# Kernel optimization log

Measured on AMD Instinct MI355X. Metric: run time of the kernel, lower is better.

Reference implementation:

```python
import jax, jax.numpy as jnp
import numpy as np

N = 100000   # nodes per graph-set
E = 600000   # edges
G = 64       # graphs in batch
H = 128      # hidden size (atom_h == voro_h == embeddings)
STEPS = 4
F_B = 90     # atom feature length
F_V = 20     # voro feature length


def setup_inputs() -> dict:
    key = jax.random.key(0)
    ks = jax.random.split(key, 16)
    inp = {
        "x_b": jax.random.uniform(ks[0], (N, F_B), dtype=jnp.float32),
        "edge_index_b": jax.random.randint(ks[1], (2, E), 0, N, dtype=jnp.int32),
        "batch_b": jnp.sort(jax.random.randint(ks[2], (N,), 0, G, dtype=jnp.int32)),
        "x_v": jax.random.uniform(ks[3], (N, F_V), dtype=jnp.float32),
        "edge_index_v": jax.random.randint(ks[4], (2, E), 0, N, dtype=jnp.int32),
        "batch_v": jnp.sort(jax.random.randint(ks[5], (N,), 0, G, dtype=jnp.int32)),
        # embedding linears (bias=False)
        "W_emb_b": jax.random.normal(ks[6], (F_B, H), dtype=jnp.float32) * 0.05,
        "W_emb_v": jax.random.normal(ks[7], (F_V, H), dtype=jnp.float32) * 0.05,
        # GatedGraphConv (the *bond* block — source applies it to both graphs)
        "ggc_weight": jax.random.normal(ks[8], (STEPS, H, H), dtype=jnp.float32) * 0.05,
        "gru_w_ih": jax.random.normal(ks[9], (3 * H, H), dtype=jnp.float32) * 0.05,
        "gru_w_hh": jax.random.normal(ks[10], (3 * H, H), dtype=jnp.float32) * 0.05,
        "gru_b_ih": jnp.zeros((3 * H,), dtype=jnp.float32),
        "gru_b_hh": jnp.zeros((3 * H,), dtype=jnp.float32),
        # output block (hidden = 2H)
        "W1": jax.random.normal(ks[11], (2 * H, 2 * H), dtype=jnp.float32) * 0.05,
        "b1": jnp.zeros((2 * H,), dtype=jnp.float32),
        "W2": jax.random.normal(ks[12], (2 * H, 1), dtype=jnp.float32) * 0.05,
        "b2": jnp.zeros((1,), dtype=jnp.float32),
    }
    return inp


def _gru_cell(m, h, w_ih, w_hh, b_ih, b_hh):
    gi = m @ w_ih.T + b_ih   # [N, 3H]
    gh = h @ w_hh.T + b_hh
    i_r, i_z, i_n = jnp.split(gi, 3, axis=-1)
    h_r, h_z, h_n = jnp.split(gh, 3, axis=-1)
    r = jax.nn.sigmoid(i_r + h_r)
    z = jax.nn.sigmoid(i_z + h_z)
    n = jnp.tanh(i_n + r * h_n)
    return (1.0 - z) * n + z * h


def _gated_graph_conv(x, edge_index, ggc_weight, gru_w_ih, gru_w_hh, gru_b_ih, gru_b_hh):
    # x: [N, H] (in_channels == out_channels, no padding needed)
    src, dst = edge_index[0], edge_index[1]
    h = x
    for i in range(STEPS):
        m = h @ ggc_weight[i]                                   # [N, H]
        agg = jax.ops.segment_sum(m[src], dst, num_segments=N)  # add-aggregation
        h = _gru_cell(agg, h, gru_w_ih, gru_w_hh, gru_b_ih, gru_b_hh)
    return h


def _mean_pool(x, batch):
    sums = jax.ops.segment_sum(x, batch, num_segments=G)
    cnt = jax.ops.segment_sum(jnp.ones((x.shape[0],), x.dtype), batch, num_segments=G)
    return sums / jnp.maximum(cnt, 1.0)[:, None]


def reference(x_b, edge_index_b, batch_b, x_v, edge_index_v, batch_v,
              W_emb_b, W_emb_v, ggc_weight, gru_w_ih, gru_w_hh, gru_b_ih, gru_b_hh,
              W1, b1, W2, b2):
    # embedding blocks: relu(linear(x)) (no bias)
    hb = jax.nn.relu(x_b @ W_emb_b)
    hv = jax.nn.relu(x_v @ W_emb_v)
    # NOTE: source (faithfully) applies mpnn_layer_bond to BOTH graphs
    hb = _gated_graph_conv(hb, edge_index_b, ggc_weight, gru_w_ih, gru_w_hh, gru_b_ih, gru_b_hh)
    hv = _gated_graph_conv(hv, edge_index_v, ggc_weight, gru_w_ih, gru_w_hh, gru_b_ih, gru_b_hh)
    gb = _mean_pool(jax.nn.relu(hb), batch_b)   # [G, H]
    gv = _mean_pool(jax.nn.relu(hv), batch_v)   # [G, H]
    g = jnp.concatenate([gb, gv], axis=1)       # [G, 2H]
    out = jax.nn.softplus(jax.nn.relu(g @ W1 + b1) @ W2 + b2)
    return out.squeeze(1)                       # [G]
```

## Files before the change

### kernel.cpp

```cpp
#include <hip/hip_runtime.h>
#include <hip/hip_bf16.h>
#include <math.h>

#define N_NODES   100000
#define N_EDGES   600000
#define NG        64
#define H         128
#define STEPS     4
#define FB        90
#define FV        20
#define NN        (2*N_NODES)
#define EE        (2*N_EDGES)
#define BSTR      40
#define NBLK      196
#define NNP       (NBLK*1024)

#define WCAT_KC   (12*64*8)
#define WCAT_HALF (8*WCAT_KC)
#define WCAT_STEP (2*WCAT_HALF)

typedef unsigned short u16;
typedef __attribute__((ext_vector_type(8))) __bf16 bf16x8;
typedef __attribute__((ext_vector_type(4))) float  floatx4;

static __device__ __forceinline__ float bf16_lo(unsigned u){ return __uint_as_float(u << 16); }
static __device__ __forceinline__ float bf16_hi(unsigned u){ return __uint_as_float(u & 0xffff0000u); }
static __device__ __forceinline__ u16 f2bf(float f){
    union { float f; unsigned u; } v; v.f = f;
    unsigned r = v.u + 0x7fffu + ((v.u >> 16) & 1u);
    return (u16)(r >> 16);
}
static __device__ __forceinline__ float fastrcp(float x){ return __builtin_amdgcn_rcpf(x); }
static __device__ __forceinline__ float fsigmoid(float x){ return fastrcp(1.f + __expf(-x)); }
static __device__ __forceinline__ float ftanh(float x){ return 1.f - 2.f*fastrcp(1.f + __expf(2.f*x)); }


__global__ void deg_kernel(const int* __restrict__ eib, const int* __restrict__ eiv,
                           int* __restrict__ deg){
    int e = blockIdx.x*blockDim.x + threadIdx.x;
    if (e >= EE) return;
    int d;
    if (e < N_EDGES) d = eib[N_EDGES + e];
    else             d = eiv[N_EDGES + (e - N_EDGES)] + N_NODES;
    atomicAdd(&deg[d], 1);
}

__global__ __launch_bounds__(256) void bsum_kernel(const int* __restrict__ deg, int* __restrict__ bsum){
    int t = threadIdx.x;
    int4 v = reinterpret_cast<const int4*>(deg)[blockIdx.x*256 + t];
    int s = v.x + v.y + v.z + v.w;
    __shared__ int ss[256];
    ss[t] = s; __syncthreads();
    for (int off = 128; off > 0; off >>= 1){ if (t < off) ss[t] += ss[t + off]; __syncthreads(); }
    if (t == 0) bsum[blockIdx.x] = ss[0];
}

__global__ __launch_bounds__(256) void bscan_kernel(const int* __restrict__ bsum, int* __restrict__ boff){
    int t = threadIdx.x;
    int v = (t < NBLK) ? bsum[t] : 0;
    __shared__ int ss[256];
    ss[t] = v; __syncthreads();
    for (int off = 1; off < 256; off <<= 1){
        int u = (t >= off) ? ss[t - off] : 0;
        __syncthreads();
        ss[t] += u;
        __syncthreads();
    }
    boff[t] = ss[t] - v;
}

__global__ __launch_bounds__(256) void scan_final_kernel(const int* __restrict__ deg, const int* __restrict__ boff,
                                                         int* __restrict__ row_ptr, int* __restrict__ cursor){
    int t = threadIdx.x, b = blockIdx.x;
    int4 v = reinterpret_cast<const int4*>(deg)[b*256 + t];
    int s = v.x + v.y + v.z + v.w;
    __shared__ int ss[256];
    ss[t] = s; __syncthreads();
    for (int off = 1; off < 256; off <<= 1){
        int u = (t >= off) ? ss[t - off] : 0;
        __syncthreads();
        ss[t] += u;
        __syncthreads();
    }
    int base = boff[b] + ss[t] - s;
    int i0 = b*1024 + t*4;
    int e0 = base, e1 = e0 + v.x, e2 = e1 + v.y, e3 = e2 + v.z;
    if (i0 < NN){
        int4 w = make_int4(e0, e1, e2, e3);
        reinterpret_cast<int4*>(row_ptr)[i0 >> 2] = w;
        reinterpret_cast<int4*>(cursor)[i0 >> 2]  = w;
    }
    if (b == 0 && t == 0) row_ptr[NN] = EE;
}

__global__ void csr_fill_kernel(const int* __restrict__ eib, const int* __restrict__ eiv,
                                int* __restrict__ cursor, int* __restrict__ csr_src){
    int e = blockIdx.x*blockDim.x + threadIdx.x;
    if (e >= EE) return;
    int s, d;
    if (e < N_EDGES){ s = eib[e];                 d = eib[N_EDGES + e]; }
    else { int e2 = e - N_EDGES; s = eiv[e2] + N_NODES; d = eiv[N_EDGES + e2] + N_NODES; }
    int pos = atomicAdd(&cursor[d], 1);
    csr_src[pos] = s;
}

__global__ __launch_bounds__(128) void fold_kernel(const float* __restrict__ ggc_w,
                                                   const float* __restrict__ w_ih,
                                                   float* __restrict__ Bfold){
    int blk = blockIdx.x;
    int s = blk >> 7, k = blk & 127;
    __shared__ float wg[128];
    int t = threadIdx.x;
    wg[t] = ggc_w[(size_t)s*H*H + (size_t)k*H + t];
    __syncthreads();
    for (int c = t; c < 384; c += 128){
        const float* wr = w_ih + (size_t)c*H;
        float acc = 0.f;
        for (int q = 0; q < 128; q += 4){
            float4 a = *reinterpret_cast<const float4*>(&wg[q]);
            float4 b = *reinterpret_cast<const float4*>(&wr[q]);
            acc += a.x*b.x + a.y*b.y + a.z*b.z + a.w*b.w;
        }
        Bfold[((size_t)s*H + k)*384 + c] = acc;
    }
}

__global__ void pack_kernel(const float* __restrict__ Bfold, const float* __restrict__ w_hh,
                            u16* __restrict__ Wcat){
    int idx = blockIdx.x*256 + threadIdx.x;
    if (idx >= STEPS*WCAT_STEP) return;
    int v    = idx & 7;
    int lane = (idx >> 3) & 63;
    int t    = (idx >> 9) % 12;
    int rem  = idx / (512*12);
    int kc   = rem & 7;
    int b1   = (rem >> 3) & 1;
    int s    = rem >> 4;
    int col16 = lane & 15, l4 = lane >> 4;
    int k = kc*32 + l4*8 + v;
    int g = t >> 2, jj = t & 3;
    int c = (4*b1 + jj)*16 + col16;
    int gc = (g == 2) ? (256 + c) : (g*128 + c);
    float val;
    if (k < 128) val = Bfold[((size_t)s*H + k)*384 + gc];
    else         val = w_hh[(size_t)gc*H + (k - 128)];
    Wcat[idx] = f2bf(val);
}


__global__ __launch_bounds__(128) void emb_kernel(const float* __restrict__ xb, const float* __restrict__ xv,
                                                  const float* __restrict__ Wb, const float* __restrict__ Wv,
                                                  u16* __restrict__ hb){
    __shared__ float xs[8][FB];
    int j = threadIdx.x;
    int n0 = blockIdx.x * 8;
    const float* x; const float* W; int K; int xoff;
    if (n0 < N_NODES){ x = xb; W = Wb; K = FB; xoff = n0; }
    else             { x = xv; W = Wv; K = FV; xoff = n0 - N_NODES; }
    for (int i = j; i < 8*K; i += 128){ int r = i / K, c = i - r*K; xs[r][c] = x[(xoff + r)*K + c]; }
    __syncthreads();
    float acc[8];
    #pragma unroll
    for (int n = 0; n < 8; ++n) acc[n] = 0.f;
    for (int k = 0; k < K; ++k){
        float w = W[k*H + j];
        #pragma unroll
        for (int n = 0; n < 8; ++n) acc[n] = fmaf(xs[n][k], w, acc[n]);
    }
    #pragma unroll
    for (int n = 0; n < 8; ++n)
        hb[(size_t)(n0 + n)*H + j] = f2bf(fmaxf(acc[n], 0.f));
}


__global__ __launch_bounds__(256) void agg_kernel(const u16* __restrict__ hb,
                                                  const int* __restrict__ row_ptr,
                                                  const int* __restrict__ csr_src,
                                                  u16* __restrict__ aggb){
    int wid  = threadIdx.x >> 6;
    int lane = threadIdx.x & 63;
    int q    = lane >> 4;
    int c    = lane & 15;
    int node = blockIdx.x*4 + wid;
    int beg = row_ptr[node], end = row_ptr[node+1];
    const uint4* rows = reinterpret_cast<const uint4*>(hb);
    float s0=0.f,s1=0.f,s2=0.f,s3=0.f,s4=0.f,s5=0.f,s6=0.f,s7=0.f;
    float u0=0.f,u1=0.f,u2=0.f,u3=0.f,u4=0.f,u5=0.f,u6=0.f,u7=0.f;
    int e = beg + q;
    for (; e + 4 < end; e += 8){
        int sA = csr_src[e];
        int sB = csr_src[e + 4];
        uint4 a = rows[(size_t)sA*16 + c];
        uint4 b = rows[(size_t)sB*16 + c];
        s0 += bf16_lo(a.x); s1 += bf16_hi(a.x); s2 += bf16_lo(a.y); s3 += bf16_hi(a.y);
        s4 += bf16_lo(a.z); s5 += bf16_hi(a.z); s6 += bf16_lo(a.w); s7 += bf16_hi(a.w);
        u0 += bf16_lo(b.x); u1 += bf16_hi(b.x); u2 += bf16_lo(b.y); u3 += bf16_hi(b.y);
        u4 += bf16_lo(b.z); u5 += bf16_hi(b.z); u6 += bf16_lo(b.w); u7 += bf16_hi(b.w);
    }
    if (e < end){
        int sA = csr_src[e];
        uint4 a = rows[(size_t)sA*16 + c];
        s0 += bf16_lo(a.x); s1 += bf16_hi(a.x); s2 += bf16_lo(a.y); s3 += bf16_hi(a.y);
        s4 += bf16_lo(a.z); s5 += bf16_hi(a.z); s6 += bf16_lo(a.w); s7 += bf16_hi(a.w);
    }
    s0 += u0; s1 += u1; s2 += u2; s3 += u3; s4 += u4; s5 += u5; s6 += u6; s7 += u7;
    s0 += __shfl_xor(s0, 16); s1 += __shfl_xor(s1, 16); s2 += __shfl_xor(s2, 16); s3 += __shfl_xor(s3, 16);
    s4 += __shfl_xor(s4, 16); s5 += __shfl_xor(s5, 16); s6 += __shfl_xor(s6, 16); s7 += __shfl_xor(s7, 16);
    s0 += __shfl_xor(s0, 32); s1 += __shfl_xor(s1, 32); s2 += __shfl_xor(s2, 32); s3 += __shfl_xor(s3, 32);
    s4 += __shfl_xor(s4, 32); s5 += __shfl_xor(s5, 32); s6 += __shfl_xor(s6, 32); s7 += __shfl_xor(s7, 32);
    if (q == 0){
        uint4 o;
        o.x = (unsigned)f2bf(s0) | ((unsigned)f2bf(s1) << 16);
        o.y = (unsigned)f2bf(s2) | ((unsigned)f2bf(s3) << 16);
        o.z = (unsigned)f2bf(s4) | ((unsigned)f2bf(s5) << 16);
        o.w = (unsigned)f2bf(s6) | ((unsigned)f2bf(s7) << 16);
        reinterpret_cast<uint4*>(aggb)[(size_t)node*16 + c] = o;
    }
}


__global__ __launch_bounds__(256, 3) void gru_mfma_kernel(const u16* __restrict__ aggb,
                                                          const u16* __restrict__ hb_in,
                                                          u16* __restrict__ hb_out,
                                                          const u16* __restrict__ Wcat,
                                                          const float* __restrict__ b_ih,
                                                          const float* __restrict__ b_hh){
    __shared__ u16 Bs[WCAT_KC];
    __shared__ u16 As[64*BSTR];
    const int t = threadIdx.x;
    const int wid = t >> 6, lane = t & 63;
    const int l15 = lane & 15, l4 = lane >> 4;
    const int n0 = blockIdx.x * 64;
    const int b1 = blockIdx.y;
    const u16* Wsrc = Wcat + (size_t)b1*WCAT_HALF;

    floatx4 accR[4], accZ[4], accNi[4], accNh[4];
    #pragma unroll
    for (int i = 0; i < 4; ++i){
        accR[i] = (floatx4){0.f,0.f,0.f,0.f};  accZ[i]  = (floatx4){0.f,0.f,0.f,0.f};
        accNi[i] = (floatx4){0.f,0.f,0.f,0.f}; accNh[i] = (floatx4){0.f,0.f,0.f,0.f};
    }

    for (int kc = 0; kc < 8; ++kc){
        __syncthreads();
        {
            const u16* src = Wsrc + (size_t)kc*WCAT_KC;
#if __has_builtin(__builtin_amdgcn_global_load_lds)
            #pragma unroll
            for (int p = 0; p < 3; ++p){
                int i = t + p*256;
                __builtin_amdgcn_global_load_lds(
                    (const __attribute__((address_space(1))) void*)(src + (size_t)i*8),
                    (__attribute__((address_space(3))) void*)(&Bs[i*8]), 16, 0, 0);
            }
#else
            #pragma unroll
            for (int p = 0; p < 3; ++p){
                int i = t + p*256;
                *reinterpret_cast<int4*>(&Bs[i*8]) = *reinterpret_cast<const int4*>(src + (size_t)i*8);
            }
#endif
        }
        {
            int row = t >> 2, part = t & 3;
            const u16* srcA = (kc < 4) ? aggb : hb_in;
            const int4 v = *reinterpret_cast<const int4*>(srcA + (size_t)(n0 + row)*H + (kc & 3)*32 + part*8);
            *reinterpret_cast<int4*>(&As[row*BSTR + part*8]) = v;
        }
        __syncthreads();
        bf16x8 aF = *reinterpret_cast<const bf16x8*>(&As[(wid*16 + l15)*BSTR + l4*8]);
        if (kc < 4){
            #pragma unroll
            for (int j = 0; j < 4; ++j){
                bf16x8 bR = *reinterpret_cast<const bf16x8*>(&Bs[((0*4 + j)*64 + lane)*8]);
                bf16x8 bZ = *reinterpret_cast<const bf16x8*>(&Bs[((1*4 + j)*64 + lane)*8]);
                bf16x8 bN = *reinterpret_cast<const bf16x8*>(&Bs[((2*4 + j)*64 + lane)*8]);
                accR[j]  = __builtin_amdgcn_mfma_f32_16x16x32_bf16(aF, bR, accR[j], 0, 0, 0);
                accZ[j]  = __builtin_amdgcn_mfma_f32_16x16x32_bf16(aF, bZ, accZ[j], 0, 0, 0);
                accNi[j] = __builtin_amdgcn_mfma_f32_16x16x32_bf16(aF, bN, accNi[j], 0, 0, 0);
            }
        } else {
            #pragma unroll
            for (int j = 0; j < 4; ++j){
                bf16x8 bR = *reinterpret_cast<const bf16x8*>(&Bs[((0*4 + j)*64 + lane)*8]);
                bf16x8 bZ = *reinterpret_cast<const bf16x8*>(&Bs[((1*4 + j)*64 + lane)*8]);
                bf16x8 bN = *reinterpret_cast<const bf16x8*>(&Bs[((2*4 + j)*64 + lane)*8]);
                accR[j]  = __builtin_amdgcn_mfma_f32_16x16x32_bf16(aF, bR, accR[j], 0, 0, 0);
                accZ[j]  = __builtin_amdgcn_mfma_f32_16x16x32_bf16(aF, bZ, accZ[j], 0, 0, 0);
                accNh[j] = __builtin_amdgcn_mfma_f32_16x16x32_bf16(aF, bN, accNh[j], 0, 0, 0);
            }
        }
    }

    const int rowb = n0 + wid*16 + l4*4;
    #pragma unroll
    for (int jj = 0; jj < 4; ++jj){
        int col = (4*b1 + jj)*16 + l15;
        float br  = b_ih[col]       + b_hh[col];
        float bz  = b_ih[128 + col] + b_hh[128 + col];
        float bin = b_ih[256 + col];
        float bhn = b_hh[256 + col];
        #pragma unroll
        for (int rg = 0; rg < 4; ++rg){
            int row = rowb + rg;
            float r   = fsigmoid(accR[jj][rg] + br);
            float z   = fsigmoid(accZ[jj][rg] + bz);
            float nn_ = ftanh(accNi[jj][rg] + bin + r*(accNh[jj][rg] + bhn));
            float hold = bf16_lo((unsigned)hb_in[(size_t)row*H + col]);
            float hnew = (1.f - z)*nn_ + z*hold;
            hb_out[(size_t)row*H + col] = f2bf(hnew);
        }
    }
}


__global__ __launch_bounds__(128) void pool_kernel(const u16* __restrict__ hb,
                                                   const int* __restrict__ batch_b, const int* __restrict__ batch_v,
                                                   float* __restrict__ pool){
    int j  = threadIdx.x;
    int n0 = blockIdx.x * 32;
    bool voro = (n0 >= N_NODES);
    int colbase = voro ? 128 : 0;
    int gcur = -1; float acc = 0.f;
    for (int r = 0; r < 32; ++r){
        int node = n0 + r;
        int g = voro ? batch_v[node - N_NODES] : batch_b[node];
        if (g != gcur){
            if (gcur >= 0) atomicAdd(&pool[gcur*256 + colbase + j], acc);
            acc = 0.f; gcur = g;
        }
        acc += fmaxf(bf16_lo((unsigned)hb[(size_t)node*H + j]), 0.f);
    }
    if (gcur >= 0) atomicAdd(&pool[gcur*256 + colbase + j], acc);
}

__global__ __launch_bounds__(256) void cnt_kernel(const int* __restrict__ batch_b, const int* __restrict__ batch_v,
                                                  int* __restrict__ cnt){
    __shared__ int bins[128];
    int t = threadIdx.x;
    if (t < 128) bins[t] = 0;
    __syncthreads();
    int i = blockIdx.x*256 + t;
    if (i < NN){
        int g = (i < N_NODES) ? batch_b[i] : 64 + batch_v[i - N_NODES];
        atomicAdd(&bins[g], 1);
    }
    __syncthreads();
    if (t < 128 && bins[t] > 0) atomicAdd(&cnt[t], bins[t]);
}


__global__ __launch_bounds__(256) void head_kernel(const float* __restrict__ pool, const int* __restrict__ cnt,
                                                   const float* __restrict__ W1, const float* __restrict__ b1,
                                                   const float* __restrict__ W2, const float* __restrict__ b2,
                                                   float* __restrict__ out){
    __shared__ float gs[256];
    __shared__ float wsum[4];
    int b = blockIdx.x, j = threadIdx.x;
    int c = (j < 128) ? cnt[b] : cnt[64 + b];
    float denom = (float)((c > 1) ? c : 1);
    gs[j] = pool[b*256 + j] / denom;
    __syncthreads();
    float acc = b1[j];
    for (int k = 0; k < 256; ++k) acc = fmaf(gs[k], W1[k*256 + j], acc);
    float y = fmaxf(acc, 0.f) * W2[j];
    #pragma unroll
    for (int off = 32; off > 0; off >>= 1) y += __shfl_down(y, off, 64);
    if ((j & 63) == 0) wsum[j >> 6] = y;
    __syncthreads();
    if (j == 0){
        float x = wsum[0] + wsum[1] + wsum[2] + wsum[3] + b2[0];
        float sp = (x > 0.f) ? x + log1pf(expf(-x)) : log1pf(expf(x));
        out[b] = sp;
    }
}


extern "C" void kernel_launch(void* const* d_in, const int* in_sizes, int n_in,
                              void* d_out, int out_size, void* d_ws, size_t ws_size,
                              hipStream_t stream){
    const float* x_b      = (const float*)d_in[0];
    const int*   eib      = (const int*)  d_in[1];
    const int*   batch_b  = (const int*)  d_in[2];
    const float* x_v      = (const float*)d_in[3];
    const int*   eiv      = (const int*)  d_in[4];
    const int*   batch_v  = (const int*)  d_in[5];
    const float* W_emb_b  = (const float*)d_in[6];
    const float* W_emb_v  = (const float*)d_in[7];
    const float* ggc_w    = (const float*)d_in[8];
    const float* gru_w_ih = (const float*)d_in[9];
    const float* gru_w_hh = (const float*)d_in[10];
    const float* gru_b_ih = (const float*)d_in[11];
    const float* gru_b_hh = (const float*)d_in[12];
    const float* W1       = (const float*)d_in[13];
    const float* b1       = (const float*)d_in[14];
    const float* W2       = (const float*)d_in[15];
    const float* b2       = (const float*)d_in[16];
    float* out = (float*)d_out;

    char* ws = (char*)d_ws;
    size_t off = 0;
    auto alloc = [&](size_t bytes)->char*{
        char* p = ws + off; off += (bytes + 255)/256*256; return p;
    };
    u16*   hb0      = (u16*)   alloc((size_t)NN*H*2);
    u16*   hb1      = (u16*)   alloc((size_t)NN*H*2);
    u16*   aggb     = (u16*)   alloc((size_t)NN*H*2);
    float* Bfold    = (float*) alloc((size_t)STEPS*H*384*4);
    u16*   Wcat     = (u16*)   alloc((size_t)STEPS*WCAT_STEP*2);
    int*   row_ptr  = (int*)   alloc((size_t)(NN+1)*4);
    int*   deg      = (int*)   alloc((size_t)NNP*4);
    int*   cursor   = (int*)   alloc((size_t)NN*4);
    int*   csr_src  = (int*)   alloc((size_t)EE*4);
    int*   bsum     = (int*)   alloc((size_t)256*4);
    int*   boff     = (int*)   alloc((size_t)256*4);
    float* pool     = (float*) alloc((size_t)NG*2*H*4);
    int*   cnt      = (int*)   alloc((size_t)2*NG*4);
    (void)ws_size; (void)in_sizes; (void)n_in; (void)out_size;

    hipMemsetAsync(deg,  0, (size_t)NNP*4, stream);
    hipMemsetAsync(pool, 0, (size_t)NG*2*H*4, stream);
    hipMemsetAsync(cnt,  0, (size_t)2*NG*4, stream);

    deg_kernel        <<<(EE + 255)/256, 256, 0, stream>>>(eib, eiv, deg);
    bsum_kernel       <<<NBLK, 256, 0, stream>>>(deg, bsum);
    bscan_kernel      <<<1, 256, 0, stream>>>(bsum, boff);
    scan_final_kernel <<<NBLK, 256, 0, stream>>>(deg, boff, row_ptr, cursor);
    csr_fill_kernel   <<<(EE + 255)/256, 256, 0, stream>>>(eib, eiv, cursor, csr_src);
    fold_kernel       <<<STEPS*H, 128, 0, stream>>>(ggc_w, gru_w_ih, Bfold);
    pack_kernel       <<<(STEPS*WCAT_STEP + 255)/256, 256, 0, stream>>>(Bfold, gru_w_hh, Wcat);

    emb_kernel<<<NN/8, 128, 0, stream>>>(x_b, x_v, W_emb_b, W_emb_v, hb0);

    u16* hbs[2] = { hb0, hb1 };
    for (int s = 0; s < STEPS; ++s){
        u16* hin  = hbs[s & 1];
        u16* hout = hbs[(s + 1) & 1];
        agg_kernel     <<<NN/4, 256, 0, stream>>>(hin, row_ptr, csr_src, aggb);
        gru_mfma_kernel<<<dim3(NN/64, 2), 256, 0, stream>>>(aggb, hin, hout,
                                                            Wcat + (size_t)s*WCAT_STEP,
                                                            gru_b_ih, gru_b_hh);
    }

    pool_kernel<<<NN/32, 128, 0, stream>>>(hb0, batch_b, batch_v, pool);
    cnt_kernel <<<(NN + 255)/256, 256, 0, stream>>>(batch_b, batch_v, cnt);
    head_kernel<<<NG, 256, 0, stream>>>(pool, cnt, W1, b1, W2, b2, out);
}
```

Baseline: 955.7 us.

## Fuse neighbor aggregation into GRU MFMA kernel via shared memory

```diff
diff --git a/kernel.cpp b/kernel.cpp
--- a/kernel.cpp
+++ b/kernel.cpp
@@ -11,9 +11,9 @@
 #define FV        20
 #define NN        (2*N_NODES)
 #define EE        (2*N_EDGES)
-#define BSTR      40
 #define NBLK      196
 #define NNP       (NBLK*1024)
+#define AGSTR     136
 
 #define WCAT_KC   (12*64*8)
 #define WCAT_HALF (8*WCAT_KC)
@@ -173,66 +173,72 @@
 }
 
 
-__global__ __launch_bounds__(256) void agg_kernel(const u16* __restrict__ hb,
-                                                  const int* __restrict__ row_ptr,
-                                                  const int* __restrict__ csr_src,
-                                                  u16* __restrict__ aggb){
-    int wid  = threadIdx.x >> 6;
-    int lane = threadIdx.x & 63;
-    int q    = lane >> 4;
-    int c    = lane & 15;
-    int node = blockIdx.x*4 + wid;
-    int beg = row_ptr[node], end = row_ptr[node+1];
-    const uint4* rows = reinterpret_cast<const uint4*>(hb);
-    float s0=0.f,s1=0.f,s2=0.f,s3=0.f,s4=0.f,s5=0.f,s6=0.f,s7=0.f;
-    float u0=0.f,u1=0.f,u2=0.f,u3=0.f,u4=0.f,u5=0.f,u6=0.f,u7=0.f;
-    int e = beg + q;
-    for (; e + 4 < end; e += 8){
-        int sA = csr_src[e];
-        int sB = csr_src[e + 4];
-        uint4 a = rows[(size_t)sA*16 + c];
-        uint4 b = rows[(size_t)sB*16 + c];
-        s0 += bf16_lo(a.x); s1 += bf16_hi(a.x); s2 += bf16_lo(a.y); s3 += bf16_hi(a.y);
-        s4 += bf16_lo(a.z); s5 += bf16_hi(a.z); s6 += bf16_lo(a.w); s7 += bf16_hi(a.w);
-        u0 += bf16_lo(b.x); u1 += bf16_hi(b.x); u2 += bf16_lo(b.y); u3 += bf16_hi(b.y);
-        u4 += bf16_lo(b.z); u5 += bf16_hi(b.z); u6 += bf16_lo(b.w); u7 += bf16_hi(b.w);
-    }
-    if (e < end){
-        int sA = csr_src[e];
-        uint4 a = rows[(size_t)sA*16 + c];
-        s0 += bf16_lo(a.x); s1 += bf16_hi(a.x); s2 += bf16_lo(a.y); s3 += bf16_hi(a.y);
-        s4 += bf16_lo(a.z); s5 += bf16_hi(a.z); s6 += bf16_lo(a.w); s7 += bf16_hi(a.w);
-    }
-    s0 += u0; s1 += u1; s2 += u2; s3 += u3; s4 += u4; s5 += u5; s6 += u6; s7 += u7;
-    s0 += __shfl_xor(s0, 16); s1 += __shfl_xor(s1, 16); s2 += __shfl_xor(s2, 16); s3 += __shfl_xor(s3, 16);
-    s4 += __shfl_xor(s4, 16); s5 += __shfl_xor(s5, 16); s6 += __shfl_xor(s6, 16); s7 += __shfl_xor(s7, 16);
-    s0 += __shfl_xor(s0, 32); s1 += __shfl_xor(s1, 32); s2 += __shfl_xor(s2, 32); s3 += __shfl_xor(s3, 32);
-    s4 += __shfl_xor(s4, 32); s5 += __shfl_xor(s5, 32); s6 += __shfl_xor(s6, 32); s7 += __shfl_xor(s7, 32);
-    if (q == 0){
-        uint4 o;
-        o.x = (unsigned)f2bf(s0) | ((unsigned)f2bf(s1) << 16);
-        o.y = (unsigned)f2bf(s2) | ((unsigned)f2bf(s3) << 16);
-        o.z = (unsigned)f2bf(s4) | ((unsigned)f2bf(s5) << 16);
-        o.w = (unsigned)f2bf(s6) | ((unsigned)f2bf(s7) << 16);
-        reinterpret_cast<uint4*>(aggb)[(size_t)node*16 + c] = o;
-    }
-}
-
-
-__global__ __launch_bounds__(256, 3) void gru_mfma_kernel(const u16* __restrict__ aggb,
-                                                          const u16* __restrict__ hb_in,
-                                                          u16* __restrict__ hb_out,
-                                                          const u16* __restrict__ Wcat,
-                                                          const float* __restrict__ b_ih,
-                                                          const float* __restrict__ b_hh){
-    __shared__ u16 Bs[WCAT_KC];
-    __shared__ u16 As[64*BSTR];
+__global__ __launch_bounds__(512, 4) void step_kernel(const u16* __restrict__ hb_in,
+                                                      u16* __restrict__ hb_out,
+                                                      const int* __restrict__ row_ptr,
+                                                      const int* __restrict__ csr_src,
+                                                      const u16* __restrict__ Wcat,
+                                                      const float* __restrict__ b_ih,
+                                                      const float* __restrict__ b_hh){
+    __shared__ u16 AggS[64*AGSTR];
+    __shared__ u16 HbS [64*AGSTR];
+    __shared__ u16 Bs  [2*WCAT_KC];
     const int t = threadIdx.x;
     const int wid = t >> 6, lane = t & 63;
     const int l15 = lane & 15, l4 = lane >> 4;
+    const int w4  = wid & 3;
+    const int b1h = wid >> 2;
     const int n0 = blockIdx.x * 64;
-    const int b1 = blockIdx.y;
-    const u16* Wsrc = Wcat + (size_t)b1*WCAT_HALF;
+
+    {
+        #pragma unroll
+        for (int p = 0; p < 2; ++p){
+            int i = t + p*512;
+            int row = i >> 4, part = i & 15;
+            const int4 v = *reinterpret_cast<const int4*>(hb_in + (size_t)(n0 + row)*H + part*8);
+            *reinterpret_cast<int4*>(&HbS[row*AGSTR + part*8]) = v;
+        }
+    }
+    {
+        int q = lane >> 4, c = lane & 15;
+        const uint4* rows = reinterpret_cast<const uint4*>(hb_in);
+        for (int it = 0; it < 8; ++it){
+            int node = n0 + wid*8 + it;
+            int beg = row_ptr[node], end = row_ptr[node+1];
+            float s0=0.f,s1=0.f,s2=0.f,s3=0.f,s4=0.f,s5=0.f,s6=0.f,s7=0.f;
+            float u0=0.f,u1=0.f,u2=0.f,u3=0.f,u4=0.f,u5=0.f,u6=0.f,u7=0.f;
+            int e = beg + q;
+            for (; e + 4 < end; e += 8){
+                int sA = csr_src[e];
+                int sB = csr_src[e + 4];
+                uint4 a = rows[(size_t)sA*16 + c];
+                uint4 b = rows[(size_t)sB*16 + c];
+                s0 += bf16_lo(a.x); s1 += bf16_hi(a.x); s2 += bf16_lo(a.y); s3 += bf16_hi(a.y);
+                s4 += bf16_lo(a.z); s5 += bf16_hi(a.z); s6 += bf16_lo(a.w); s7 += bf16_hi(a.w);
+                u0 += bf16_lo(b.x); u1 += bf16_hi(b.x); u2 += bf16_lo(b.y); u3 += bf16_hi(b.y);
+                u4 += bf16_lo(b.z); u5 += bf16_hi(b.z); u6 += bf16_lo(b.w); u7 += bf16_hi(b.w);
+            }
+            if (e < end){
+                int sA = csr_src[e];
+                uint4 a = rows[(size_t)sA*16 + c];
+                s0 += bf16_lo(a.x); s1 += bf16_hi(a.x); s2 += bf16_lo(a.y); s3 += bf16_hi(a.y);
+                s4 += bf16_lo(a.z); s5 += bf16_hi(a.z); s6 += bf16_lo(a.w); s7 += bf16_hi(a.w);
+            }
+            s0 += u0; s1 += u1; s2 += u2; s3 += u3; s4 += u4; s5 += u5; s6 += u6; s7 += u7;
+            s0 += __shfl_xor(s0, 16); s1 += __shfl_xor(s1, 16); s2 += __shfl_xor(s2, 16); s3 += __shfl_xor(s3, 16);
+            s4 += __shfl_xor(s4, 16); s5 += __shfl_xor(s5, 16); s6 += __shfl_xor(s6, 16); s7 += __shfl_xor(s7, 16);
+            s0 += __shfl_xor(s0, 32); s1 += __shfl_xor(s1, 32); s2 += __shfl_xor(s2, 32); s3 += __shfl_xor(s3, 32);
+            s4 += __shfl_xor(s4, 32); s5 += __shfl_xor(s5, 32); s6 += __shfl_xor(s6, 32); s7 += __shfl_xor(s7, 32);
+            if (q == 0){
+                uint4 o;
+                o.x = (unsigned)f2bf(s0) | ((unsigned)f2bf(s1) << 16);
+                o.y = (unsigned)f2bf(s2) | ((unsigned)f2bf(s3) << 16);
+                o.z = (unsigned)f2bf(s4) | ((unsigned)f2bf(s5) << 16);
+                o.w = (unsigned)f2bf(s6) | ((unsigned)f2bf(s7) << 16);
+                *reinterpret_cast<uint4*>(&AggS[(wid*8 + it)*AGSTR + c*8]) = o;
+            }
+        }
+    }
 
     floatx4 accR[4], accZ[4], accNi[4], accNh[4];
     #pragma unroll
@@ -244,37 +250,36 @@
     for (int kc = 0; kc < 8; ++kc){
         __syncthreads();
         {
-            const u16* src = Wsrc + (size_t)kc*WCAT_KC;
+            const u16* src = Wcat + (size_t)kc*WCAT_KC;
 #if __has_builtin(__builtin_amdgcn_global_load_lds)
             #pragma unroll
             for (int p = 0; p < 3; ++p){
-                int i = t + p*256;
+                int i = t + p*512;
+                int half = (i >= 768), idx = i - half*768;
                 __builtin_amdgcn_global_load_lds(
-                    (const __attribute__((address_space(1))) void*)(src + (size_t)i*8),
-                    (__attribute__((address_space(3))) void*)(&Bs[i*8]), 16, 0, 0);
+                    (const __attribute__((address_space(1))) void*)(src + (size_t)half*WCAT_HALF + (size_t)idx*8),
+                    (__attribute__((address_space(3))) void*)(&Bs[(half*768 + idx)*8]), 16, 0, 0);
             }
 #else
             #pragma unroll
             for (int p = 0; p < 3; ++p){
-                int i = t + p*256;
-                *reinterpret_cast<int4*>(&Bs[i*8]) = *reinterpret_cast<const int4*>(src + (size_t)i*8);
+                int i = t + p*512;
+                int half = (i >= 768), idx = i - half*768;
+                *reinterpret_cast<int4*>(&Bs[(half*768 + idx)*8]) =
+                    *reinterpret_cast<const int4*>(src + (size_t)half*WCAT_HALF + (size_t)idx*8);
             }
 #endif
         }
-        {
-            int row = t >> 2, part = t & 3;
-            const u16* srcA = (kc < 4) ? aggb : hb_in;
-            const int4 v = *reinterpret_cast<const int4*>(srcA + (size_t)(n0 + row)*H + (kc & 3)*32 + part*8);
-            *reinterpret_cast<int4*>(&As[row*BSTR + part*8]) = v;
-        }
-        __syncthreads();
-        bf16x8 aF = *reinterpret_cast<const bf16x8*>(&As[(wid*16 + l15)*BSTR + l4*8]);
+        __syncthreads();
+        const u16* Asrc = (kc < 4) ? AggS : HbS;
+        bf16x8 aF = *reinterpret_cast<const bf16x8*>(&Asrc[(w4*16 + l15)*AGSTR + (kc & 3)*32 + l4*8]);
+        const u16* Bh = &Bs[b1h*WCAT_KC];
         if (kc < 4){
             #pragma unroll
             for (int j = 0; j < 4; ++j){
-                bf16x8 bR = *reinterpret_cast<const bf16x8*>(&Bs[((0*4 + j)*64 + lane)*8]);
-                bf16x8 bZ = *reinterpret_cast<const bf16x8*>(&Bs[((1*4 + j)*64 + lane)*8]);
-                bf16x8 bN = *reinterpret_cast<const bf16x8*>(&Bs[((2*4 + j)*64 + lane)*8]);
+                bf16x8 bR = *reinterpret_cast<const bf16x8*>(&Bh[((0*4 + j)*64 + lane)*8]);
+                bf16x8 bZ = *reinterpret_cast<const bf16x8*>(&Bh[((1*4 + j)*64 + lane)*8]);
+                bf16x8 bN = *reinterpret_cast<const bf16x8*>(&Bh[((2*4 + j)*64 + lane)*8]);
                 accR[j]  = __builtin_amdgcn_mfma_f32_16x16x32_bf16(aF, bR, accR[j], 0, 0, 0);
                 accZ[j]  = __builtin_amdgcn_mfma_f32_16x16x32_bf16(aF, bZ, accZ[j], 0, 0, 0);
                 accNi[j] = __builtin_amdgcn_mfma_f32_16x16x32_bf16(aF, bN, accNi[j], 0, 0, 0);
@@ -282,9 +287,9 @@
         } else {
             #pragma unroll
             for (int j = 0; j < 4; ++j){
-                bf16x8 bR = *reinterpret_cast<const bf16x8*>(&Bs[((0*4 + j)*64 + lane)*8]);
-                bf16x8 bZ = *reinterpret_cast<const bf16x8*>(&Bs[((1*4 + j)*64 + lane)*8]);
-                bf16x8 bN = *reinterpret_cast<const bf16x8*>(&Bs[((2*4 + j)*64 + lane)*8]);
+                bf16x8 bR = *reinterpret_cast<const bf16x8*>(&Bh[((0*4 + j)*64 + lane)*8]);
+                bf16x8 bZ = *reinterpret_cast<const bf16x8*>(&Bh[((1*4 + j)*64 + lane)*8]);
+                bf16x8 bN = *reinterpret_cast<const bf16x8*>(&Bh[((2*4 + j)*64 + lane)*8]);
                 accR[j]  = __builtin_amdgcn_mfma_f32_16x16x32_bf16(aF, bR, accR[j], 0, 0, 0);
                 accZ[j]  = __builtin_amdgcn_mfma_f32_16x16x32_bf16(aF, bZ, accZ[j], 0, 0, 0);
                 accNh[j] = __builtin_amdgcn_mfma_f32_16x16x32_bf16(aF, bN, accNh[j], 0, 0, 0);
@@ -292,10 +297,10 @@
         }
     }
 
-    const int rowb = n0 + wid*16 + l4*4;
+    const int rowb = n0 + w4*16 + l4*4;
     #pragma unroll
     for (int jj = 0; jj < 4; ++jj){
-        int col = (4*b1 + jj)*16 + l15;
+        int col = (4*b1h + jj)*16 + l15;
         float br  = b_ih[col]       + b_hh[col];
         float bz  = b_ih[128 + col] + b_hh[128 + col];
         float bin = b_ih[256 + col];
@@ -306,7 +311,7 @@
             float r   = fsigmoid(accR[jj][rg] + br);
             float z   = fsigmoid(accZ[jj][rg] + bz);
             float nn_ = ftanh(accNi[jj][rg] + bin + r*(accNh[jj][rg] + bhn));
-            float hold = bf16_lo((unsigned)hb_in[(size_t)row*H + col]);
+            float hold = bf16_lo((unsigned)HbS[(row - n0)*AGSTR + col]);
             float hnew = (1.f - z)*nn_ + z*hold;
             hb_out[(size_t)row*H + col] = f2bf(hnew);
         }
@@ -405,7 +410,6 @@
     };
     u16*   hb0      = (u16*)   alloc((size_t)NN*H*2);
     u16*   hb1      = (u16*)   alloc((size_t)NN*H*2);
-    u16*   aggb     = (u16*)   alloc((size_t)NN*H*2);
     float* Bfold    = (float*) alloc((size_t)STEPS*H*384*4);
     u16*   Wcat     = (u16*)   alloc((size_t)STEPS*WCAT_STEP*2);
     int*   row_ptr  = (int*)   alloc((size_t)(NN+1)*4);
@@ -436,10 +440,9 @@
     for (int s = 0; s < STEPS; ++s){
         u16* hin  = hbs[s & 1];
         u16* hout = hbs[(s + 1) & 1];
-        agg_kernel     <<<NN/4, 256, 0, stream>>>(hin, row_ptr, csr_src, aggb);
-        gru_mfma_kernel<<<dim3(NN/64, 2), 256, 0, stream>>>(aggb, hin, hout,
-                                                            Wcat + (size_t)s*WCAT_STEP,
-                                                            gru_b_ih, gru_b_hh);
+        step_kernel<<<NN/64, 512, 0, stream>>>(hin, hout, row_ptr, csr_src,
+                                               Wcat + (size_t)s*WCAT_STEP,
+                                               gru_b_ih, gru_b_hh);
     }
 
     pool_kernel<<<NN/32, 128, 0, stream>>>(hb0, batch_b, batch_v, pool);
```

New measurement: 1.011 ms. 1.06x slower.
